# Kernel optimization log

Hardware: AMD Instinct MI355X
Metric: run time of the kernel (lower is better)

## Reference

```python
import jax, jax.numpy as jnp
import numpy as np

T, B, P, D = 64, 32, 9, 512  # turns, batch, parties(=N_s), D_u=D_k=D_h


def setup_inputs() -> dict:
    key = jax.random.key(0)
    ks = jax.random.split(key, 12)
    f = lambda k, s: jax.random.normal(k, s, dtype=jnp.float32)
    sc = 0.02
    spk = jax.random.randint(ks[5], (T, B), 0, P)
    return {
        "U": f(ks[0], (T, B, D)), "SK": f(ks[1], (T, B, D)),
        "NU": f(ks[2], (T, B, D)), "LK": f(ks[3], (T, B, D)),
        "A": f(ks[4], (T, B, D)),
        "qmask": jax.nn.one_hot(spk, P, dtype=jnp.float32),  # one-hot party mask [T,B,P]
        # 4 Attention blocks (state11,state12,state21,state22): w_k, w_q, proj (D->D each)
        "Wk": f(ks[6], (4, D, D)) * sc, "bk": jnp.zeros((4, D), jnp.float32),
        "Wq": f(ks[7], (4, D, D)) * sc, "bq": jnp.zeros((4, D), jnp.float32),
        "Wp": f(ks[8], (4, D, D)) * sc, "bp": jnp.zeros((4, D), jnp.float32),
        # per-speaker GRUCell weights (dict of GRUCells -> stacked [P, ...], torch gate order r,z,n)
        "Wih": f(ks[9], (P, 3 * D, D)) * sc, "Whh": f(ks[10], (P, 3 * D, D)) * sc,
        "bih": jnp.zeros((P, 3 * D), jnp.float32), "bhh": jnp.zeros((P, 3 * D), jnp.float32),
    }


def reference(U, SK, NU, LK, A, qmask, Wk, bk, Wq, bq, Wp, bp, Wih, Whh, bih, bhh):
    Tn, Bn, Dn = U.shape
    Pn = qmask.shape[-1]
    bidx = jnp.arange(Bn)

    def attn(i, k2, q2):
        # Attention(D_k), n_head=1, score_function='dot_product', dropout=0 (eval)
        kx = k2 @ Wk[i].T + bk[i]                 # [B, D]
        qx = q2 @ Wq[i].T + bq[i]                 # [B, D]
        # k_len=q_len=1 -> score = <qx_b, kx_b>; original softmaxes over dim=0 (the batch axis!)
        score = jax.nn.softmax(jnp.sum(qx * kx, axis=-1), axis=0)  # [B]
        return (score[:, None] * kx) @ Wp[i].T + bp[i]  # [B, D]

    def gru(x, h, idx):
        # dynamically-routed per-speaker GRUCell: gather speaker weights, batched matvec
        gi = jnp.einsum('bd,bkd->bk', x, Wih[idx]) + bih[idx]  # [B, 3D]
        gh = jnp.einsum('bd,bkd->bk', h, Whh[idx]) + bhh[idx]
        ir, iz, inn = jnp.split(gi, 3, axis=-1)
        hr, hz, hn = jnp.split(gh, 3, axis=-1)
        r = jax.nn.sigmoid(ir + hr)
        z = jax.nn.sigmoid(iz + hz)
        n = jnp.tanh(inn + r * hn)
        return (1.0 - z) * n + z * h

    # qmask_n[t] = qmask[t+1] (next speaker), last repeats
    qmask_n = jnp.concatenate([qmask[1:], qmask[-1:]], axis=0)

    def step(s, xs):
        u, sk, nu, lk, qm, qmn = xs
        qi = jnp.argmax(qm, axis=1)   # speaker id per sample
        qni = jnp.argmax(qmn, axis=1)  # listener (next speaker) id
        s0s = s[bidx, qi]              # _select_parties
        s0l = s[bidx, qni]
        s_0 = attn(0, sk, u)
        s_s = attn(1, sk, s_0)
        s_1 = attn(2, lk, nu)
        s_l = attn(3, lk, s_1)
        spk = gru(s_s, s0s, qi)        # speaker state update
        lst = gru(s_l, s0l, qni)       # listener state update
        s_full = jnp.zeros_like(s).at[bidx, qi].set(spk)   # scatter_ dim=1
        l_full = jnp.zeros_like(s).at[bidx, qni].set(lst)
        s_new = (s * (1.0 - qm[..., None] - qmn[..., None])
                 + s_full * qm[..., None] + l_full * qmn[..., None])
        return s_new, s_new[bidx, qi]  # emit selected speaker state

    s0 = jnp.zeros((Bn, Pn, Dn), U.dtype)
    _, outs = jax.lax.scan(step, s0, (U, SK, NU, LK, qmask, qmask_n))
    # s_ starts as zeros(1, B, D_h) and concatenates per-step selections -> [T+1, B, D]
    return jnp.concatenate([jnp.zeros((1, Bn, Dn), U.dtype), outs], axis=0)
```

## Files before the change

kernel.cpp:

```cpp
#include <hip/hip_runtime.h>
#include <math.h>

#define Tn 64
#define Bn 32
#define Pn 9
#define Dn 512
#define TBn 2048
#define G3 1536
#define NCH 16
#define DD2 262144

using short8 = __attribute__((ext_vector_type(8))) short;
using f32x4  = __attribute__((ext_vector_type(4))) float;
typedef unsigned long long ull;
typedef unsigned int uint;

__device__ __forceinline__ float fsigmoid(float x){ return 1.0f/(1.0f+__expf(-x)); }
__device__ __forceinline__ ushort f2bf(float x){
  unsigned u = __float_as_uint(x);
  return (ushort)((u + 0x7FFFu + ((u>>16)&1u)) >> 16);
}
__device__ __forceinline__ float bf2f(ushort h){
  return __uint_as_float(((unsigned)h)<<16);
}
__device__ __forceinline__ uint pk32(float x){
  ushort h = f2bf(x);
  ushort l = f2bf(x - bf2f(h));
  return ((uint)h << 16) | (uint)l;
}

__device__ __forceinline__ ull ld_agent8(const ull* p){
  return __hip_atomic_load(p, __ATOMIC_RELAXED, __HIP_MEMORY_SCOPE_AGENT);
}
__device__ __forceinline__ void st_agent8(ull* p, ull v){
  __hip_atomic_store(p, v, __ATOMIC_RELAXED, __HIP_MEMORY_SCOPE_AGENT);
}
__device__ __forceinline__ unsigned ld_agent4(const int* p){
  return (unsigned)__hip_atomic_load(p, __ATOMIC_RELAXED, __HIP_MEMORY_SCOPE_AGENT);
}
__device__ __forceinline__ void st_agent4(int* p, int v){
  __hip_atomic_store(p, v, __ATOMIC_RELAXED, __HIP_MEMORY_SCOPE_AGENT);
}
__device__ __forceinline__ float ulo(ull v){ return __uint_as_float((unsigned)v); }
__device__ __forceinline__ float uhi(ull v){ return __uint_as_float((unsigned)(v>>32)); }
__device__ __forceinline__ ull upack(float a, float b){
  return ((ull)__float_as_uint(b) << 32) | (ull)__float_as_uint(a);
}
__device__ __forceinline__ float wave_red(float a){
  a += __shfl_xor(a, 1);  a += __shfl_xor(a, 2);  a += __shfl_xor(a, 4);
  a += __shfl_xor(a, 8);  a += __shfl_xor(a, 16); a += __shfl_xor(a, 32);
  return a;
}

__global__ void k_prep(const float* __restrict__ qmask, int* __restrict__ qi,
                       int* __restrict__ qni, float* __restrict__ h0A,
                       float* __restrict__ h0B, float* __restrict__ out,
                       int* __restrict__ counts, int* __restrict__ lists,
                       int* __restrict__ dcnt, int* __restrict__ dlist,
                       int* __restrict__ rowflag){
  int t = blockIdx.x; int tid = threadIdx.x;
  int gidx = blockIdx.x*256 + tid;
  if (gidx < 16) counts[gidx] = 0;
  if (gidx < Bn*Pn*NCH) st_agent4(&rowflag[gidx], 0);
  for (int i=gidx; i<9*4096; i+=64*256) lists[i] = -1;
  __shared__ int qis[32], qnis[32];
  __shared__ int cnt9[9];
  if (tid < 9) cnt9[tid] = 0;
  if (tid < Bn){
    int b = tid;
    const float* qm = qmask + ((size_t)t*Bn + b)*Pn;
    int best = 0; float bv = qm[0];
    #pragma unroll
    for (int p=1;p<Pn;p++){ float v=qm[p]; if (v>bv){bv=v;best=p;} }
    qi[t*Bn+b] = best; qis[b] = best;
    int tn = (t==Tn-1)? t : t+1;
    const float* qmn = qmask + ((size_t)tn*Bn + b)*Pn;
    best = 0; bv = qmn[0];
    #pragma unroll
    for (int p=1;p<Pn;p++){ float v=qmn[p]; if (v>bv){bv=v;best=p;} }
    qni[t*Bn+b] = best; qnis[b] = best;
  }
  __syncthreads();
  if (tid < Bn){
    int sp = qis[tid], lp = qnis[tid];
    if (sp == lp){
      int i = atomicAdd(&cnt9[sp], 1);
      dlist[(t*9+sp)*32 + i] = tid | 256 | 512;
    } else {
      int i = atomicAdd(&cnt9[sp], 1);
      dlist[(t*9+sp)*32 + i] = tid | 256;
      int j = atomicAdd(&cnt9[lp], 1);
      dlist[(t*9+lp)*32 + j] = tid | 512;
    }
  }
  __syncthreads();
  if (tid < 9) dcnt[t*9+tid] = cnt9[tid];
  for (int i=tid; i<2304; i+=256){ h0A[t*2304 + i] = 0.f; h0B[t*2304 + i] = 0.f; }
  for (int i=tid; i<256;  i+=256) out[t*256 + i] = 0.f;
}

__global__ __launch_bounds__(256) void k_aux(
    const int* __restrict__ qi, const int* __restrict__ qni,
    int* __restrict__ counts, int* __restrict__ lists,
    const int* __restrict__ dcnt, int* __restrict__ dlist,
    const float* __restrict__ Wq, const float* __restrict__ Wih,
    const float* __restrict__ Wp, const float* __restrict__ bp,
    const float* __restrict__ bq, const float* __restrict__ bih,
    ushort* __restrict__ WpTpk, float* __restrict__ cvec,
    float* __restrict__ C1, float* __restrict__ C3){
  int bx = blockIdx.x, tid = threadIdx.x;
  if (bx < 16){
    int id = bx*256 + tid;
    int role = id >> 11, tb = id & (TBn-1);
    int p = role ? qni[tb] : qi[tb];
    int slot = atomicAdd(&counts[p], 1);
    lists[p*4096 + slot] = id;
  } else if (bx == 16){
    for (int idx = tid; idx < Bn*Pn; idx += 256){
      int b = idx / Pn, pp = idx % Pn;
      int v = 0;
      for (int t=0;t<Tn;t++){
        if (qi[t*Bn+b]==pp || qni[t*Bn+b]==pp){
          int nn = dcnt[t*9+pp];
          int base = (t*9+pp)*32;
          for (int i=0;i<nn;i++){
            if ((dlist[base+i] & 31) == b){ dlist[base+i] |= (v<<16); break; }
          }
          v++;
        }
      }
    }
  } else if (bx < 33){
    int g = (bx-17)*256 + tid;
    int r = g >> 3, cb = (g & 7)*64;
    #pragma unroll
    for (int mi=0; mi<2; mi++){
      const float* src = Wp + (size_t)mi*2*DD2;
      ushort* dst = WpTpk + (size_t)(mi*512 + r)*1024;
      for (int c=cb; c<cb+64; c++){
        float v = src[(size_t)c*512 + r];
        ushort h = f2bf(v);
        dst[c] = h; dst[512+c] = f2bf(v - bf2f(h));
      }
    }
  } else {
    int wv = (bx-33)*4 + (tid>>6), lane = tid & 63;
    if (wv < 16){
      for (int i=0;i<64;i++){
        int r = wv*64 + i;
        int m = r >> 9, j = r & 511;
        const float* wrow = Wq + (size_t)(m?3:1)*DD2 + (size_t)j*512;
        const float* bpv  = bp + (m? 1024 : 0);
        float acc = 0.f;
        #pragma unroll
        for (int e=0;e<8;e++) acc = fmaf(wrow[lane*8+e], bpv[lane*8+e], acc);
        acc = wave_red(acc);
        if (lane==0) cvec[r] = acc + bq[(m?1536:512) + j];
      }
    } else if (wv < 232){
      int base = (wv-16)*64;
      for (int i=0;i<64;i++){
        int r = base + i;
        const float* wrow = Wih + (size_t)r*512;
        float a1=0.f, a3=0.f;
        #pragma unroll
        for (int e=0;e<8;e++){
          float wv8 = wrow[lane*8+e];
          a1 = fmaf(wv8, bp[512 + lane*8+e], a1);
          a3 = fmaf(wv8, bp[1536 + lane*8+e], a3);
        }
        a1 = wave_red(a1); a3 = wave_red(a3);
        if (lane==0){ C1[r] = a1 + bih[r]; C3[r] = a3 + bih[r]; }
      }
    }
  }
}

struct PkD { const float* s; ushort* d; int n; };
__global__ __launch_bounds__(256) void k_packB(PkD p0, PkD p1, PkD p2, PkD p3,
                                               PkD p4, PkD p5, PkD p6, PkD p7){
  PkD D;
  switch (blockIdx.z){
    case 0: D=p0; break; case 1: D=p1; break; case 2: D=p2; break; case 3: D=p3; break;
    case 4: D=p4; break; case 5: D=p5; break; case 6: D=p6; break; default: D=p7; break;
  }
  int total = D.n * 128;
  for (int idx = blockIdx.x*256 + threadIdx.x; idx < total; idx += gridDim.x*256){
    int r = idx >> 7, c4 = idx & 127;
    float4 v = ((const float4*)D.s)[idx];
    ushort h0=f2bf(v.x), h1=f2bf(v.y), h2=f2bf(v.z), h3=f2bf(v.w);
    ushort l0=f2bf(v.x-bf2f(h0)), l1=f2bf(v.y-bf2f(h1)),
           l2=f2bf(v.z-bf2f(h2)), l3=f2bf(v.w-bf2f(h3));
    ushort* base = D.d + (size_t)r*1024;
    *(ushort4*)(base + c4*4)       = make_ushort4(h0,h1,h2,h3);
    *(ushort4*)(base + 512 + c4*4) = make_ushort4(l0,l1,l2,l3);
  }
}

struct MMd {
  const ushort* A; const ushort* B; float* C; const float* bias; ushort* Cpk;
  int asr, ahi, alo, bsr, bhi, blo, ldc, gx;
};
__global__ __launch_bounds__(256) void k_mmB(MMd d0, MMd d1, MMd d2, MMd d3){
  MMd d;
  switch (blockIdx.z){
    case 0: d=d0; break; case 1: d=d1; break; case 2: d=d2; break; default: d=d3; break;
  }
  if ((int)blockIdx.x >= d.gx) return;
  __shared__ ushort AshH[64*64];
  __shared__ ushort AshL[64*64];
  __shared__ ushort BshH[64*64];
  __shared__ ushort BshL[64*64];
  int bm = blockIdx.y*64, bn = blockIdx.x*64;
  int tid = threadIdx.x;
  int lane = tid & 63, w = tid >> 6;
  int wm = (w>>1)*32, wn = (w&1)*32;
  f32x4 acc[2][2] = {};
  int r0 = tid >> 3, g0 = tid & 7;
  int r1 = r0 + 32;
  const ushort* Ah = d.A + d.ahi;
  const ushort* Al = d.A + d.alo;
  const ushort* Bh = d.B + d.bhi;
  const ushort* Bl = d.B + d.blo;
  for (int k0=0; k0<512; k0+=64){
    short8 vah0 = *(const short8*)(Ah + (size_t)(bm+r0)*d.asr + k0 + g0*8);
    short8 vah1 = *(const short8*)(Ah + (size_t)(bm+r1)*d.asr + k0 + g0*8);
    short8 val0 = *(const short8*)(Al + (size_t)(bm+r0)*d.asr + k0 + g0*8);
    short8 val1 = *(const short8*)(Al + (size_t)(bm+r1)*d.asr + k0 + g0*8);
    short8 vbh0 = *(const short8*)(Bh + (size_t)(bn+r0)*d.bsr + k0 + g0*8);
    short8 vbh1 = *(const short8*)(Bh + (size_t)(bn+r1)*d.bsr + k0 + g0*8);
    short8 vbl0 = *(const short8*)(Bl + (size_t)(bn+r0)*d.bsr + k0 + g0*8);
    short8 vbl1 = *(const short8*)(Bl + (size_t)(bn+r1)*d.bsr + k0 + g0*8);
    __syncthreads();
    *(short8*)(AshH + r0*64 + ((g0 ^ (r0&7))*8)) = vah0;
    *(short8*)(AshH + r1*64 + ((g0 ^ (r1&7))*8)) = vah1;
    *(short8*)(AshL + r0*64 + ((g0 ^ (r0&7))*8)) = val0;
    *(short8*)(AshL + r1*64 + ((g0 ^ (r1&7))*8)) = val1;
    *(short8*)(BshH + r0*64 + ((g0 ^ (r0&7))*8)) = vbh0;
    *(short8*)(BshH + r1*64 + ((g0 ^ (r1&7))*8)) = vbh1;
    *(short8*)(BshL + r0*64 + ((g0 ^ (r0&7))*8)) = vbl0;
    *(short8*)(BshL + r1*64 + ((g0 ^ (r1&7))*8)) = vbl1;
    __syncthreads();
    #pragma unroll
    for (int kk=0; kk<2; ++kk){
      int gs = kk*4 + (lane>>4);
      short8 afh[2], afl[2], bfh[2], bfl[2];
      #pragma unroll
      for (int mi=0; mi<2; ++mi){
        int row = wm + mi*16 + (lane&15);
        afh[mi] = *(const short8*)(AshH + row*64 + ((gs ^ (row&7))*8));
        afl[mi] = *(const short8*)(AshL + row*64 + ((gs ^ (row&7))*8));
      }
      #pragma unroll
      for (int ni=0; ni<2; ++ni){
        int row = wn + ni*16 + (lane&15);
        bfh[ni] = *(const short8*)(BshH + row*64 + ((gs ^ (row&7))*8));
        bfl[ni] = *(const short8*)(BshL + row*64 + ((gs ^ (row&7))*8));
      }
      #pragma unroll
      for (int mi=0; mi<2; ++mi)
        #pragma unroll
        for (int ni=0; ni<2; ++ni){
          acc[mi][ni] = __builtin_amdgcn_mfma_f32_16x16x32_bf16(afh[mi], bfh[ni], acc[mi][ni], 0,0,0);
          acc[mi][ni] = __builtin_amdgcn_mfma_f32_16x16x32_bf16(afh[mi], bfl[ni], acc[mi][ni], 0,0,0);
          acc[mi][ni] = __builtin_amdgcn_mfma_f32_16x16x32_bf16(afl[mi], bfh[ni], acc[mi][ni], 0,0,0);
        }
    }
  }
  #pragma unroll
  for (int mi=0; mi<2; ++mi){
    #pragma unroll
    for (int ni=0; ni<2; ++ni){
      #pragma unroll
      for (int i=0;i<4;i++){
        int row = bm + wm + mi*16 + (lane>>4)*4 + i;
        int col = bn + wn + ni*16 + (lane&15);
        float v = acc[mi][ni][i];
        if (d.bias) v += d.bias[col];
        if (d.C) d.C[(size_t)row*d.ldc + col] = v;
        if (d.Cpk){
          ushort h = f2bf(v);
          d.Cpk[(size_t)row*2*d.ldc + col] = h;
          d.Cpk[(size_t)row*2*d.ldc + d.ldc + col] = f2bf(v - bf2f(h));
        }
      }
    }
  }
}

__global__ __launch_bounds__(256) void k_mm_g(
    const ushort* __restrict__ Spk0, const ushort* __restrict__ Spk1,
    const ushort* __restrict__ Wihpk,
    const int* __restrict__ counts, const int* __restrict__ lists,
    float* __restrict__ gis, float* __restrict__ gil)
{
  int p = blockIdx.z;
  int mt = blockIdx.y;
  if (mt*64 >= counts[p]) return;
  int bn = blockIdx.x*64;
  __shared__ ushort AshH[64*64];
  __shared__ ushort AshL[64*64];
  __shared__ ushort BshH[64*64];
  __shared__ ushort BshL[64*64];
  __shared__ int rid[64];
  int tid = threadIdx.x;
  int lane = tid & 63, w = tid >> 6;
  int wm = (w>>1)*32, wn = (w&1)*32;
  if (tid < 64) rid[tid] = lists[p*4096 + mt*64 + tid];
  __syncthreads();
  f32x4 acc[2][2] = {};
  int r0 = tid >> 3, g0 = tid & 7;
  int r1 = r0 + 32;
  int id0 = rid[r0], id1 = rid[r1];
  const ushort* As0 = (id0 >= 0) ? (((id0>>11)? Spk1:Spk0) + (size_t)(id0 & (TBn-1))*1024) : nullptr;
  const ushort* As1 = (id1 >= 0) ? (((id1>>11)? Spk1:Spk0) + (size_t)(id1 & (TBn-1))*1024) : nullptr;
  const ushort* Wb  = Wihpk + (size_t)(p*G3 + bn)*1024;
  short8 zz = {0,0,0,0,0,0,0,0};
  for (int k0=0; k0<512; k0+=64){
    short8 vah0 = As0 ? *(const short8*)(As0 + k0 + g0*8)       : zz;
    short8 val0 = As0 ? *(const short8*)(As0 + 512 + k0 + g0*8) : zz;
    short8 vah1 = As1 ? *(const short8*)(As1 + k0 + g0*8)       : zz;
    short8 val1 = As1 ? *(const short8*)(As1 + 512 + k0 + g0*8) : zz;
    short8 vbh0 = *(const short8*)(Wb + (size_t)r0*1024 + k0 + g0*8);
    short8 vbl0 = *(const short8*)(Wb + (size_t)r0*1024 + 512 + k0 + g0*8);
    short8 vbh1 = *(const short8*)(Wb + (size_t)r1*1024 + k0 + g0*8);
    short8 vbl1 = *(const short8*)(Wb + (size_t)r1*1024 + 512 + k0 + g0*8);
    __syncthreads();
    *(short8*)(AshH + r0*64 + ((g0 ^ (r0&7))*8)) = vah0;
    *(short8*)(AshH + r1*64 + ((g0 ^ (r1&7))*8)) = vah1;
    *(short8*)(AshL + r0*64 + ((g0 ^ (r0&7))*8)) = val0;
    *(short8*)(AshL + r1*64 + ((g0 ^ (r1&7))*8)) = val1;
    *(short8*)(BshH + r0*64 + ((g0 ^ (r0&7))*8)) = vbh0;
    *(short8*)(BshH + r1*64 + ((g0 ^ (r1&7))*8)) = vbh1;
    *(short8*)(BshL + r0*64 + ((g0 ^ (r0&7))*8)) = vbl0;
    *(short8*)(BshL + r1*64 + ((g0 ^ (r1&7))*8)) = vbl1;
    __syncthreads();
    #pragma unroll
    for (int kk=0; kk<2; ++kk){
      int gs = kk*4 + (lane>>4);
      short8 afh[2], afl[2], bfh[2], bfl[2];
      #pragma unroll
      for (int mi=0; mi<2; ++mi){
        int row = wm + mi*16 + (lane&15);
        afh[mi] = *(const short8*)(AshH + row*64 + ((gs ^ (row&7))*8));
        afl[mi] = *(const short8*)(AshL + row*64 + ((gs ^ (row&7))*8));
      }
      #pragma unroll
      for (int ni=0; ni<2; ++ni){
        int row = wn + ni*16 + (lane&15);
        bfh[ni] = *(const short8*)(BshH + row*64 + ((gs ^ (row&7))*8));
        bfl[ni] = *(const short8*)(BshL + row*64 + ((gs ^ (row&7))*8));
      }
      #pragma unroll
      for (int mi=0; mi<2; ++mi)
        #pragma unroll
        for (int ni=0; ni<2; ++ni){
          acc[mi][ni] = __builtin_amdgcn_mfma_f32_16x16x32_bf16(afh[mi], bfh[ni], acc[mi][ni], 0,0,0);
          acc[mi][ni] = __builtin_amdgcn_mfma_f32_16x16x32_bf16(afh[mi], bfl[ni], acc[mi][ni], 0,0,0);
          acc[mi][ni] = __builtin_amdgcn_mfma_f32_16x16x32_bf16(afl[mi], bfh[ni], acc[mi][ni], 0,0,0);
        }
    }
  }
  #pragma unroll
  for (int mi=0; mi<2; ++mi){
    #pragma unroll
    for (int ni=0; ni<2; ++ni){
      #pragma unroll
      for (int i=0;i<4;i++){
        int lrow2 = wm + mi*16 + (lane>>4)*4 + i;
        int id = rid[lrow2];
        if (id < 0) continue;
        int col = bn + wn + ni*16 + (lane&15);
        float* dst = ((id>>11) ? gil : gis) + (size_t)(id & (TBn-1))*G3;
        dst[col] = acc[mi][ni][i];
      }
    }
  }
}

__global__ __launch_bounds__(256) void k_scoreT(
    const float* __restrict__ qx0, const ushort* __restrict__ kxA,
    const float* __restrict__ qq1,
    const float* __restrict__ qx2, const ushort* __restrict__ kxB,
    const float* __restrict__ qq3,
    const float* __restrict__ cvec, float* __restrict__ scS,
    float* __restrict__ scL){
  int t = blockIdx.x, side = blockIdx.y, tid = threadIdx.x;
  const float* qx; const ushort* kx; const float* qq; const float* cv; float* sco;
  if (side==0){ qx=qx0; kx=kxA; qq=qq1; cv=cvec;     sco=scS; }
  else        { qx=qx2; kx=kxB; qq=qq3; cv=cvec+512; sco=scL; }
  __shared__ float p0[256], pA[256], pB[256];
  __shared__ float d0s[32], dAs[32], dBs[32], es[32], e1[32];
  int b = tid>>3, j = tid&7;
  const float* q   = qx + (size_t)(t*Bn+b)*Dn;
  const float* qqr = qq + (size_t)(t*Bn+b)*Dn;
  const ushort* kr = kx + (size_t)(t*Bn+b)*2048;
  float s0=0.f, sA=0.f, sB=0.f;
  for (int d=j; d<Dn; d+=8){
    float k0v = bf2f(kr[d])     + bf2f(kr[1024+d]);
    float k1v = bf2f(kr[512+d]) + bf2f(kr[1536+d]);
    s0 = fmaf(q[d],   k0v, s0);
    sA = fmaf(qqr[d], k1v, sA);
    sB = fmaf(cv[d],  k1v, sB);
  }
  p0[tid]=s0; pA[tid]=sA; pB[tid]=sB;
  __syncthreads();
  if (tid < 32){
    float a0=0,aA=0,aB=0;
    #pragma unroll
    for (int jj=0;jj<8;jj++){ a0+=p0[tid*8+jj]; aA+=pA[tid*8+jj]; aB+=pB[tid*8+jj]; }
    d0s[tid]=a0; dAs[tid]=aA; dBs[tid]=aB;
  }
  __syncthreads();
  if (tid < 32){
    float mx=d0s[0]; for(int o=1;o<32;o++) mx=fmaxf(mx,d0s[o]);
    es[tid]=__expf(d0s[tid]-mx);
  }
  __syncthreads();
  if (tid < 32){
    float sum=0; for(int o=0;o<32;o++) sum+=es[o];
    float sc0 = es[tid]/sum;
    e1[tid] = fmaf(sc0, dAs[tid], dBs[tid]);
  }
  __syncthreads();
  if (tid < 32){
    float mx=e1[0]; for(int o=1;o<32;o++) mx=fmaxf(mx,e1[o]);
    es[tid]=__expf(e1[tid]-mx);
  }
  __syncthreads();
  if (tid < 32){
    float sum=0; for(int o=0;o<32;o++) sum+=es[o];
    sco[t*Bn+tid] = es[tid]/sum;
  }
}

#define DC 32
#define NT 6
__global__ __launch_bounds__(512, 1) void k_rec(
    float* hA, float* hB,
    const int* __restrict__ dcnt, const int* __restrict__ dlist,
    const float* __restrict__ Whh, const float* __restrict__ bhh,
    const float* __restrict__ gis, const float* __restrict__ gil,
    const float* __restrict__ scS, const float* __restrict__ scL,
    const float* __restrict__ C1, const float* __restrict__ C3,
    float* __restrict__ out, int* rowflag){
  int p  = blockIdx.x;
  int ci = blockIdx.y;
  int d0 = ci * DC;
  int tid = threadIdx.x;
  int wave = tid >> 6, lane = tid & 63;

  __shared__ float4 hsh4[16][130];
  __shared__ uint   ab16[16][516];
  __shared__ float  ghs[16][97];
  __shared__ int    dls[32];
  __shared__ float  scSsh[TBn], scLsh[TBn];

  for (int i=tid; i<TBn; i+=512){ scSsh[i]=scS[i]; scLsh[i]=scL[i]; }

  short8 Bh[16], Bl[16];
  if (wave < NT){
    int wrow = wave*16 + (lane & 15);
    int grow = (wrow >> 5)*Dn + d0 + (wrow & 31);
    const float* wsrc = Whh + ((size_t)p*G3 + grow)*Dn + (lane>>4)*8;
    #pragma unroll
    for (int ks=0; ks<16; ++ks){
      float4 w0 = *(const float4*)(wsrc + ks*32);
      float4 w1 = *(const float4*)(wsrc + ks*32 + 4);
      float xs[8] = {w0.x,w0.y,w0.z,w0.w,w1.x,w1.y,w1.z,w1.w};
      #pragma unroll
      for (int j=0;j<8;j++){
        ushort hh = f2bf(xs[j]);
        Bh[ks][j] = (short)hh;
        Bl[ks][j] = (short)f2bf(xs[j] - bf2f(hh));
      }
    }
  }
  int dd0 = (tid & 15)*2, dfix = d0 + dd0;
  float bhr0 = bhh[p*G3 + dfix],        bhr1 = bhh[p*G3 + dfix + 1];
  float bhz0 = bhh[p*G3 + Dn + dfix],   bhz1 = bhh[p*G3 + Dn + dfix + 1];
  float bhn0 = bhh[p*G3 + 2*Dn + dfix], bhn1 = bhh[p*G3 + 2*Dn + dfix + 1];
  float c1v[6], c3v[6];
  {
    const float* C1p = C1 + p*G3; const float* C3p = C3 + p*G3;
    c1v[0]=C1p[dfix];        c1v[1]=C1p[dfix+1];
    c1v[2]=C1p[Dn+dfix];     c1v[3]=C1p[Dn+dfix+1];
    c1v[4]=C1p[2*Dn+dfix];   c1v[5]=C1p[2*Dn+dfix+1];
    c3v[0]=C3p[dfix];        c3v[1]=C3p[dfix+1];
    c3v[2]=C3p[Dn+dfix];     c3v[3]=C3p[Dn+dfix+1];
    c3v[4]=C3p[2*Dn+dfix];   c3v[5]=C3p[2*Dn+dfix+1];
  }

  int entC = 0;
  if (tid < 32) entC = dlist[(0*9 + p)*32 + tid];

  for (int t=0; t<Tn; ++t){
    __syncthreads();
    if (tid < 32) dls[tid] = entC;
    __syncthreads();
    if (t+1 < Tn && tid < 32) entC = dlist[((t+1)*9 + p)*32 + tid];
    int n = dcnt[t*9+p];
    if (!n) continue;

    float pg[12];
    {
      int i = tid >> 4;
      if (i < n && i < 16){
        int ent = dls[i]; int b = ent & 31;
        if (ent & 256){
          const float* gS = gis + (size_t)(t*Bn + b)*G3;
          pg[0]=gS[dfix]; pg[1]=gS[dfix+1]; pg[2]=gS[Dn+dfix]; pg[3]=gS[Dn+dfix+1];
          pg[4]=gS[2*Dn+dfix]; pg[5]=gS[2*Dn+dfix+1];
        }
        if (ent & 512){
          const float* gL = gil + (size_t)(t*Bn + b)*G3;
          pg[6]=gL[dfix]; pg[7]=gL[dfix+1]; pg[8]=gL[Dn+dfix]; pg[9]=gL[Dn+dfix+1];
          pg[10]=gL[2*Dn+dfix]; pg[11]=gL[2*Dn+dfix+1];
        }
      }
    }

    {
      int i0 = wave*4 + (lane >> 4);
      if (i0 < n){
        int ent = dls[i0];
        unsigned need = (unsigned)(ent >> 16);
        if (need){
          int b = ent & 31;
          const int* cell = &rowflag[(b*Pn + p)*NCH + (lane & 15)];
          while (ld_agent4(cell) < need) __builtin_amdgcn_s_sleep(1);
        }
      }
    }
    __syncthreads();

    for (int g0=0; g0<n; g0+=16){
      int gn = n - g0; if (gn > 16) gn = 16;
      for (int idx=tid; idx<gn*128; idx+=512){
        int r = idx >> 7, q = idx & 127;
        int ent = dls[g0+r];
        int b = ent & 31;
        const float* hsrc = ((ent>>16) & 1) ? hB : hA;
        const ull* src = (const ull*)(hsrc + ((size_t)b*Pn + p)*Dn) + q*2;
        ull v0 = ld_agent8(src), v1 = ld_agent8(src+1);
        float4 f; f.x = ulo(v0); f.y = uhi(v0); f.z = ulo(v1); f.w = uhi(v1);
        hsh4[r][q ^ ((q>>3)&7)] = f;
        uint4 pk; pk.x = pk32(f.x); pk.y = pk32(f.y); pk.z = pk32(f.z); pk.w = pk32(f.w);
        *(uint4*)&ab16[r][q*4] = pk;
      }
      __syncthreads();

      if (wave < NT){
        f32x4 acc = {0.f,0.f,0.f,0.f};
        int arow = lane & 15;
        int kq   = (lane >> 4)*8;
        #pragma unroll
        for (int ks=0; ks<16; ++ks){
          uint4 u0 = *(const uint4*)&ab16[arow][ks*32 + kq];
          uint4 u1 = *(const uint4*)&ab16[arow][ks*32 + kq + 4];
          uint uu[8] = {u0.x,u0.y,u0.z,u0.w,u1.x,u1.y,u1.z,u1.w};
          short8 Ah, Al;
          #pragma unroll
          for (int j=0;j<8;j++){
            Ah[j] = (short)(uu[j] >> 16);
            Al[j] = (short)(uu[j] & 0xffffu);
          }
          acc = __builtin_amdgcn_mfma_f32_16x16x32_bf16(Ah, Bh[ks], acc, 0,0,0);
          acc = __builtin_amdgcn_mfma_f32_16x16x32_bf16(Ah, Bl[ks], acc, 0,0,0);
          acc = __builtin_amdgcn_mfma_f32_16x16x32_bf16(Al, Bh[ks], acc, 0,0,0);
        }
        #pragma unroll
        for (int i=0;i<4;i++)
          ghs[(lane>>4)*4 + i][wave*16 + (lane & 15)] = acc[i];
      }
      __syncthreads();

      if (tid < gn*16){
        int i = tid >> 4;
        int ent = dls[g0+i];
        int b = ent & 31;
        bool S = (ent & 256) != 0, L = (ent & 512) != 0;
        int v = ent >> 16;
        float* hdst = (v & 1) ? hA : hB;
        int qq = dfix >> 2;
        float4 u = hsh4[i][qq ^ ((qq>>3)&7)];
        float hv0 = (dfix & 2) ? u.z : u.x;
        float hv1 = (dfix & 2) ? u.w : u.y;
        float ghr0 = ghs[i][dd0]    + bhr0, ghr1 = ghs[i][dd0+1]    + bhr1;
        float ghz0 = ghs[i][32+dd0] + bhz0, ghz1 = ghs[i][32+dd0+1] + bhz1;
        float ghn0 = ghs[i][64+dd0] + bhn0, ghn1 = ghs[i][64+dd0+1] + bhn1;
        float v0 = hv0, v1 = hv1;
        if (S){
          float g0v,g1v,g2v,g3v,g4v,g5v;
          if (g0 == 0){ g0v=pg[0]; g1v=pg[1]; g2v=pg[2]; g3v=pg[3]; g4v=pg[4]; g5v=pg[5]; }
          else {
            const float* gS = gis + (size_t)(t*Bn + b)*G3;
            g0v=gS[dfix]; g1v=gS[dfix+1]; g2v=gS[Dn+dfix]; g3v=gS[Dn+dfix+1];
            g4v=gS[2*Dn+dfix]; g5v=gS[2*Dn+dfix+1];
          }
          float sc = scSsh[t*Bn + b];
          float i0 = fmaf(sc, g0v, c1v[0]), i1 = fmaf(sc, g1v, c1v[1]);
          float i2 = fmaf(sc, g2v, c1v[2]), i3 = fmaf(sc, g3v, c1v[3]);
          float i4 = fmaf(sc, g4v, c1v[4]), i5 = fmaf(sc, g5v, c1v[5]);
          float rg0 = fsigmoid(i0 + ghr0), rg1 = fsigmoid(i1 + ghr1);
          float zg0 = fsigmoid(i2 + ghz0), zg1 = fsigmoid(i3 + ghz1);
          float ng0 = tanhf(fmaf(rg0, ghn0, i4));
          float ng1 = tanhf(fmaf(rg1, ghn1, i5));
          v0 = fmaf(zg0, hv0 - ng0, ng0);
          v1 = fmaf(zg1, hv1 - ng1, ng1);
        }
        if (L){
          float g0v,g1v,g2v,g3v,g4v,g5v;
          if (g0 == 0){ g0v=pg[6]; g1v=pg[7]; g2v=pg[8]; g3v=pg[9]; g4v=pg[10]; g5v=pg[11]; }
          else {
            const float* gL = gil + (size_t)(t*Bn + b)*G3;
            g0v=gL[dfix]; g1v=gL[dfix+1]; g2v=gL[Dn+dfix]; g3v=gL[Dn+dfix+1];
            g4v=gL[2*Dn+dfix]; g5v=gL[2*Dn+dfix+1];
          }
          float sc = scLsh[t*Bn + b];
          float i0 = fmaf(sc, g0v, c3v[0]), i1 = fmaf(sc, g1v, c3v[1]);
          float i2 = fmaf(sc, g2v, c3v[2]), i3 = fmaf(sc, g3v, c3v[3]);
          float i4 = fmaf(sc, g4v, c3v[4]), i5 = fmaf(sc, g5v, c3v[5]);
          float rg0 = fsigmoid(i0 + ghr0), rg1 = fsigmoid(i1 + ghr1);
          float zg0 = fsigmoid(i2 + ghz0), zg1 = fsigmoid(i3 + ghz1);
          float ng0 = tanhf(fmaf(rg0, ghn0, i4));
          float ng1 = tanhf(fmaf(rg1, ghn1, i5));
          float hl0 = fmaf(zg0, hv0 - ng0, ng0);
          float hl1 = fmaf(zg1, hv1 - ng1, ng1);
          if (S){ v0 += hl0 - hv0; v1 += hl1 - hv1; }
          else  { v0 = hl0; v1 = hl1; }
        }
        st_agent8((ull*)(hdst + ((size_t)b*Pn + p)*Dn + dfix), upack(v0, v1));
        if (S) *(ull*)(out + ((size_t)(t+1)*Bn + b)*Dn + dfix) = upack(v0, v1);
      }
      __syncthreads();
    }

    if (tid < n){
      int ent = dls[tid];
      st_agent4(&rowflag[((ent & 31)*Pn + p)*NCH + ci], (ent >> 16) + 1);
    }
  }
}

extern "C" void kernel_launch(void* const* d_in, const int* in_sizes, int n_in,
                              void* d_out, int out_size, void* d_ws, size_t ws_size,
                              hipStream_t stream){
  const float* U    = (const float*)d_in[0];
  const float* SK   = (const float*)d_in[1];
  const float* NU   = (const float*)d_in[2];
  const float* LK   = (const float*)d_in[3];
  const float* qmask= (const float*)d_in[5];
  const float* bk   = (const float*)d_in[7];
  const float* bq   = (const float*)d_in[9];
  const float* bp   = (const float*)d_in[11];
  const float* Wk   = (const float*)d_in[6];
  const float* Wq   = (const float*)d_in[8];
  const float* Wp   = (const float*)d_in[10];
  const float* Wih  = (const float*)d_in[12];
  const float* Whh  = (const float*)d_in[13];
  const float* bih  = (const float*)d_in[14];
  const float* bhh  = (const float*)d_in[15];
  float* out = (float*)d_out;

  char* w = (char*)d_ws;
  size_t off = 0;
  auto alloc = [&](size_t bytes)->void*{ void* p = w + off; off += (bytes + 255) & ~(size_t)255; return p; };
  ushort* SKpk  = (ushort*)alloc(2048UL*1024*2);
  ushort* LKpk  = (ushort*)alloc(2048UL*1024*2);
  ushort* Upk   = (ushort*)alloc(2048UL*1024*2);
  ushort* NUpk  = (ushort*)alloc(2048UL*1024*2);
  ushort* Wkpk  = (ushort*)alloc(2048UL*1024*2);
  ushort* Wqpk  = (ushort*)alloc(2048UL*1024*2);
  ushort* Wppk  = (ushort*)alloc(2048UL*1024*2);
  ushort* Wihpk = (ushort*)alloc(13824UL*1024*2);
  ushort* WpTpk = (ushort*)alloc(1024UL*1024*2);
  ushort* WWpk  = (ushort*)alloc(1024UL*1024*2);
  ushort* kxApk = (ushort*)alloc(2048UL*2048*2);
  ushort* kxBpk = (ushort*)alloc(2048UL*2048*2);
  ushort* pkx1pk= (ushort*)alloc(2048UL*1024*2);
  ushort* pkx3pk= (ushort*)alloc(2048UL*1024*2);
  float* qxA    = (float*)alloc(2048UL*512*4);
  float* qxB    = (float*)alloc(2048UL*512*4);
  float* qq1    = (float*)alloc(2048UL*512*4);
  float* qq3    = (float*)alloc(2048UL*512*4);
  float* gis    = (float*)alloc(2048UL*1536*4);
  float* gil    = (float*)alloc(2048UL*1536*4);
  float* hA     = (float*)alloc(32UL*9*512*4);
  float* hB     = (float*)alloc(32UL*9*512*4);
  float* cvec   = (float*)alloc(1024*4);
  float* C1     = (float*)alloc(9UL*1536*4);
  float* C3     = (float*)alloc(9UL*1536*4);
  float* scS    = (float*)alloc(2048*4);
  float* scL    = (float*)alloc(2048*4);
  int* qi       = (int*)alloc(2048*4);
  int* qni      = (int*)alloc(2048*4);
  int* counts   = (int*)alloc(16*4);
  int* lists    = (int*)alloc(9*4096*4);
  int* dcnt     = (int*)alloc(64*9*4);
  int* dlist    = (int*)alloc(64*9*32*4);
  int* rowflag  = (int*)alloc(32*9*NCH*4);
  (void)ws_size; (void)in_sizes; (void)n_in; (void)out_size;

  dim3 blk(256);

  k_prep<<<64, blk, 0, stream>>>(qmask, qi, qni, hA, hB, out, counts, lists, dcnt, dlist, rowflag);
  k_aux <<<91, blk, 0, stream>>>(qi, qni, counts, lists, dcnt, dlist,
                                 Wq, Wih, Wp, bp, bq, bih, WpTpk, cvec, C1, C3);

  {
    PkD p0{SK, SKpk, 2048}, p1{LK, LKpk, 2048}, p2{U, Upk, 2048}, p3{NU, NUpk, 2048};
    PkD p4{Wk, Wkpk, 2048}, p5{Wq, Wqpk, 2048}, p6{Wp, Wppk, 2048}, p7{Wih, Wihpk, 13824};
    k_packB<<<dim3(256,1,8), blk, 0, stream>>>(p0,p1,p2,p3,p4,p5,p6,p7);
  }

  {
    MMd d0{Wqpk+(size_t)512*1024,  WpTpk,                 nullptr, nullptr, WWpk,
           1024,0,512, 1024,0,512, 512, 8};
    MMd d1{Wqpk+(size_t)1536*1024, WpTpk+(size_t)512*1024, nullptr, nullptr, WWpk+(size_t)512*1024,
           1024,0,512, 1024,0,512, 512, 8};
    k_mmB<<<dim3(8,8,2), blk, 0, stream>>>(d0,d1,d0,d0);
  }

  {
    MMd d0{SKpk, Wkpk,                   nullptr, bk,      kxApk, 1024,0,512, 1024,0,512, 1024, 16};
    MMd d1{LKpk, Wkpk+(size_t)1024*1024, nullptr, bk+1024, kxBpk, 1024,0,512, 1024,0,512, 1024, 16};
    MMd d2{Upk,  Wqpk,                   qxA,     bq,      nullptr,1024,0,512, 1024,0,512, 512,  8};
    MMd d3{NUpk, Wqpk+(size_t)1024*1024, qxB,     bq+1024, nullptr,1024,0,512, 1024,0,512, 512,  8};
    k_mmB<<<dim3(16,32,4), blk, 0, stream>>>(d0,d1,d2,d3);
  }

  {
    MMd d0{kxApk, Wppk+(size_t)512*1024,  nullptr, nullptr, pkx1pk, 2048,512,1536, 1024,0,512, 512, 8};
    MMd d1{kxBpk, Wppk+(size_t)1536*1024, nullptr, nullptr, pkx3pk, 2048,512,1536, 1024,0,512, 512, 8};
    MMd d2{kxApk, WWpk,                   qq1,     nullptr, nullptr,2048,0,  1024, 1024,0,512, 512, 8};
    MMd d3{kxBpk, WWpk+(size_t)512*1024,  qq3,     nullptr, nullptr,2048,0,  1024, 1024,0,512, 512, 8};
    k_mmB<<<dim3(8,32,4), blk, 0, stream>>>(d0,d1,d2,d3);
  }

  k_mm_g<<<dim3(24,64,9), blk, 0, stream>>>(pkx1pk, pkx3pk, Wihpk, counts, lists, gis, gil);

  k_scoreT<<<dim3(64,2), blk, 0, stream>>>(qxA, kxApk, qq1, qxB, kxBpk, qq3, cvec, scS, scL);

  k_rec<<<dim3(9,NCH), dim3(512), 0, stream>>>(hA, hB, dcnt, dlist, Whh, bhh,
                                               gis, gil, scS, scL, C1, C3, out, rowflag);
}
```

Baseline: 653.9 us.

## Fuse activation bf16 split-packing into GEMM loads and widen aux bias precompute

Adds a GEMM variant that reads fp32 activations (SK, LK, U, NU) directly and splits them into bf16 hi/lo pairs in registers while loading tiles. This removes the separate packing pass and its workspace round-trip for those four inputs. The aux kernel's bias-folding matvecs now use one wave per row across thousands of blocks instead of 64 rows per wave over a few blocks, which raises parallelism at the cost of more block launches. The conversion is now redone by each column-block tile, so the same work is repeated redundantly.

Result: slower. 667.0 us (+2.0%).

```diff
diff --git a/kernel.cpp b/kernel.cpp
--- a/kernel.cpp
+++ b/kernel.cpp
@@ -144,45 +144,39 @@
       }
     }
   } else {
-    int wv = (bx-33)*4 + (tid>>6), lane = tid & 63;
-    if (wv < 16){
-      for (int i=0;i<64;i++){
-        int r = wv*64 + i;
-        int m = r >> 9, j = r & 511;
-        const float* wrow = Wq + (size_t)(m?3:1)*DD2 + (size_t)j*512;
-        const float* bpv  = bp + (m? 1024 : 0);
-        float acc = 0.f;
-        #pragma unroll
-        for (int e=0;e<8;e++) acc = fmaf(wrow[lane*8+e], bpv[lane*8+e], acc);
-        acc = wave_red(acc);
-        if (lane==0) cvec[r] = acc + bq[(m?1536:512) + j];
-      }
-    } else if (wv < 232){
-      int base = (wv-16)*64;
-      for (int i=0;i<64;i++){
-        int r = base + i;
-        const float* wrow = Wih + (size_t)r*512;
-        float a1=0.f, a3=0.f;
-        #pragma unroll
-        for (int e=0;e<8;e++){
-          float wv8 = wrow[lane*8+e];
-          a1 = fmaf(wv8, bp[512 + lane*8+e], a1);
-          a3 = fmaf(wv8, bp[1536 + lane*8+e], a3);
-        }
-        a1 = wave_red(a1); a3 = wave_red(a3);
-        if (lane==0){ C1[r] = a1 + bih[r]; C3[r] = a3 + bih[r]; }
-      }
+    int wid = tid >> 6, lane = tid & 63;
+    int wv = (bx-33)*4 + wid;
+    if (wv < 9*G3){
+      int r = wv;
+      const float* wrow = Wih + (size_t)r*512;
+      float a1=0.f, a3=0.f;
+      #pragma unroll
+      for (int e=0;e<8;e++){
+        float wv8 = wrow[lane*8+e];
+        a1 = fmaf(wv8, bp[512 + lane*8+e], a1);
+        a3 = fmaf(wv8, bp[1536 + lane*8+e], a3);
+      }
+      a1 = wave_red(a1); a3 = wave_red(a3);
+      if (lane==0){ C1[r] = a1 + bih[r]; C3[r] = a3 + bih[r]; }
+    } else if (wv < 9*G3 + 1024){
+      int r = wv - 9*G3;
+      int m = r >> 9, j = r & 511;
+      const float* wrow = Wq + (size_t)(m?3:1)*DD2 + (size_t)j*512;
+      const float* bpv  = bp + (m? 1024 : 0);
+      float acc = 0.f;
+      #pragma unroll
+      for (int e=0;e<8;e++) acc = fmaf(wrow[lane*8+e], bpv[lane*8+e], acc);
+      acc = wave_red(acc);
+      if (lane==0) cvec[r] = acc + bq[(m?1536:512) + j];
     }
   }
 }
 
 struct PkD { const float* s; ushort* d; int n; };
-__global__ __launch_bounds__(256) void k_packB(PkD p0, PkD p1, PkD p2, PkD p3,
-                                               PkD p4, PkD p5, PkD p6, PkD p7){
+__global__ __launch_bounds__(256) void k_packB(PkD p0, PkD p1, PkD p2, PkD p3){
   PkD D;
   switch (blockIdx.z){
-    case 0: D=p0; break; case 1: D=p1; break; case 2: D=p2; break; case 3: D=p3; break;
-    case 4: D=p4; break; case 5: D=p5; break; case 6: D=p6; break; default: D=p7; break;
+    case 0: D=p0; break; case 1: D=p1; break; case 2: D=p2; break; default: D=p3; break;
   }
   int total = D.n * 128;
   for (int idx = blockIdx.x*256 + threadIdx.x; idx < total; idx += gridDim.x*256){
@@ -227,6 +221,108 @@
     short8 vah1 = *(const short8*)(Ah + (size_t)(bm+r1)*d.asr + k0 + g0*8);
     short8 val0 = *(const short8*)(Al + (size_t)(bm+r0)*d.asr + k0 + g0*8);
     short8 val1 = *(const short8*)(Al + (size_t)(bm+r1)*d.asr + k0 + g0*8);
+    short8 vbh0 = *(const short8*)(Bh + (size_t)(bn+r0)*d.bsr + k0 + g0*8);
+    short8 vbh1 = *(const short8*)(Bh + (size_t)(bn+r1)*d.bsr + k0 + g0*8);
+    short8 vbl0 = *(const short8*)(Bl + (size_t)(bn+r0)*d.bsr + k0 + g0*8);
+    short8 vbl1 = *(const short8*)(Bl + (size_t)(bn+r1)*d.bsr + k0 + g0*8);
+    __syncthreads();
+    *(short8*)(AshH + r0*64 + ((g0 ^ (r0&7))*8)) = vah0;
+    *(short8*)(AshH + r1*64 + ((g0 ^ (r1&7))*8)) = vah1;
+    *(short8*)(AshL + r0*64 + ((g0 ^ (r0&7))*8)) = val0;
+    *(short8*)(AshL + r1*64 + ((g0 ^ (r1&7))*8)) = val1;
+    *(short8*)(BshH + r0*64 + ((g0 ^ (r0&7))*8)) = vbh0;
+    *(short8*)(BshH + r1*64 + ((g0 ^ (r1&7))*8)) = vbh1;
+    *(short8*)(BshL + r0*64 + ((g0 ^ (r0&7))*8)) = vbl0;
+    *(short8*)(BshL + r1*64 + ((g0 ^ (r1&7))*8)) = vbl1;
+    __syncthreads();
+    #pragma unroll
+    for (int kk=0; kk<2; ++kk){
+      int gs = kk*4 + (lane>>4);
+      short8 afh[2], afl[2], bfh[2], bfl[2];
+      #pragma unroll
+      for (int mi=0; mi<2; ++mi){
+        int row = wm + mi*16 + (lane&15);
+        afh[mi] = *(const short8*)(AshH + row*64 + ((gs ^ (row&7))*8));
+        afl[mi] = *(const short8*)(AshL + row*64 + ((gs ^ (row&7))*8));
+      }
+      #pragma unroll
+      for (int ni=0; ni<2; ++ni){
+        int row = wn + ni*16 + (lane&15);
+        bfh[ni] = *(const short8*)(BshH + row*64 + ((gs ^ (row&7))*8));
+        bfl[ni] = *(const short8*)(BshL + row*64 + ((gs ^ (row&7))*8));
+      }
+      #pragma unroll
+      for (int mi=0; mi<2; ++mi)
+        #pragma unroll
+        for (int ni=0; ni<2; ++ni){
+          acc[mi][ni] = __builtin_amdgcn_mfma_f32_16x16x32_bf16(afh[mi], bfh[ni], acc[mi][ni], 0,0,0);
+          acc[mi][ni] = __builtin_amdgcn_mfma_f32_16x16x32_bf16(afh[mi], bfl[ni], acc[mi][ni], 0,0,0);
+          acc[mi][ni] = __builtin_amdgcn_mfma_f32_16x16x32_bf16(afl[mi], bfh[ni], acc[mi][ni], 0,0,0);
+        }
+    }
+  }
+  #pragma unroll
+  for (int mi=0; mi<2; ++mi){
+    #pragma unroll
+    for (int ni=0; ni<2; ++ni){
+      #pragma unroll
+      for (int i=0;i<4;i++){
+        int row = bm + wm + mi*16 + (lane>>4)*4 + i;
+        int col = bn + wn + ni*16 + (lane&15);
+        float v = acc[mi][ni][i];
+        if (d.bias) v += d.bias[col];
+        if (d.C) d.C[(size_t)row*d.ldc + col] = v;
+        if (d.Cpk){
+          ushort h = f2bf(v);
+          d.Cpk[(size_t)row*2*d.ldc + col] = h;
+          d.Cpk[(size_t)row*2*d.ldc + d.ldc + col] = f2bf(v - bf2f(h));
+        }
+      }
+    }
+  }
+}
+
+struct MMf {
+  const float* A; const ushort* B; float* C; const float* bias; ushort* Cpk;
+  int asr, bsr, bhi, blo, ldc, gx;
+};
+__global__ __launch_bounds__(256) void k_mmF(MMf d0, MMf d1, MMf d2, MMf d3){
+  MMf d;
+  switch (blockIdx.z){
+    case 0: d=d0; break; case 1: d=d1; break; case 2: d=d2; break; default: d=d3; break;
+  }
+  if ((int)blockIdx.x >= d.gx) return;
+  __shared__ ushort AshH[64*64];
+  __shared__ ushort AshL[64*64];
+  __shared__ ushort BshH[64*64];
+  __shared__ ushort BshL[64*64];
+  int bm = blockIdx.y*64, bn = blockIdx.x*64;
+  int tid = threadIdx.x;
+  int lane = tid & 63, w = tid >> 6;
+  int wm = (w>>1)*32, wn = (w&1)*32;
+  f32x4 acc[2][2] = {};
+  int r0 = tid >> 3, g0 = tid & 7;
+  int r1 = r0 + 32;
+  const ushort* Bh = d.B + d.bhi;
+  const ushort* Bl = d.B + d.blo;
+  for (int k0=0; k0<512; k0+=64){
+    float4 a00 = *(const float4*)(d.A + (size_t)(bm+r0)*d.asr + k0 + g0*8);
+    float4 a01 = *(const float4*)(d.A + (size_t)(bm+r0)*d.asr + k0 + g0*8 + 4);
+    float4 a10 = *(const float4*)(d.A + (size_t)(bm+r1)*d.asr + k0 + g0*8);
+    float4 a11 = *(const float4*)(d.A + (size_t)(bm+r1)*d.asr + k0 + g0*8 + 4);
+    short8 vah0, val0, vah1, val1;
+    {
+      float xs[8] = {a00.x,a00.y,a00.z,a00.w,a01.x,a01.y,a01.z,a01.w};
+      #pragma unroll
+      for (int j=0;j<8;j++){
+        ushort h = f2bf(xs[j]); vah0[j] = (short)h; val0[j] = (short)f2bf(xs[j]-bf2f(h));
+      }
+      float ys[8] = {a10.x,a10.y,a10.z,a10.w,a11.x,a11.y,a11.z,a11.w};
+      #pragma unroll
+      for (int j=0;j<8;j++){
+        ushort h = f2bf(ys[j]); vah1[j] = (short)h; val1[j] = (short)f2bf(ys[j]-bf2f(h));
+      }
+    }
     short8 vbh0 = *(const short8*)(Bh + (size_t)(bn+r0)*d.bsr + k0 + g0*8);
     short8 vbh1 = *(const short8*)(Bh + (size_t)(bn+r1)*d.bsr + k0 + g0*8);
     short8 vbl0 = *(const short8*)(Bl + (size_t)(bn+r0)*d.bsr + k0 + g0*8);
@@ -666,10 +762,6 @@
   char* w = (char*)d_ws;
   size_t off = 0;
   auto alloc = [&](size_t bytes)->void*{ void* p = w + off; off += (bytes + 255) & ~(size_t)255; return p; };
-  ushort* SKpk  = (ushort*)alloc(2048UL*1024*2);
-  ushort* LKpk  = (ushort*)alloc(2048UL*1024*2);
-  ushort* Upk   = (ushort*)alloc(2048UL*1024*2);
-  ushort* NUpk  = (ushort*)alloc(2048UL*1024*2);
   ushort* Wkpk  = (ushort*)alloc(2048UL*1024*2);
   ushort* Wqpk  = (ushort*)alloc(2048UL*1024*2);
   ushort* Wppk  = (ushort*)alloc(2048UL*1024*2);
@@ -705,17 +797,16 @@
   dim3 blk(256);
 
   k_prep<<<64, blk, 0, stream>>>(qmask, qi, qni, hA, hB, out, counts, lists, dcnt, dlist, rowflag);
-  k_aux <<<91, blk, 0, stream>>>(qi, qni, counts, lists, dcnt, dlist,
-                                 Wq, Wih, Wp, bp, bq, bih, WpTpk, cvec, C1, C3);
+  k_aux <<<33 + 3712, blk, 0, stream>>>(qi, qni, counts, lists, dcnt, dlist,
+                                        Wq, Wih, Wp, bp, bq, bih, WpTpk, cvec, C1, C3);
 
   {
-    PkD p0{SK, SKpk, 2048}, p1{LK, LKpk, 2048}, p2{U, Upk, 2048}, p3{NU, NUpk, 2048};
-    PkD p4{Wk, Wkpk, 2048}, p5{Wq, Wqpk, 2048}, p6{Wp, Wppk, 2048}, p7{Wih, Wihpk, 13824};
-    k_packB<<<dim3(256,1,8), blk, 0, stream>>>(p0,p1,p2,p3,p4,p5,p6,p7);
+    PkD p0{Wk, Wkpk, 2048}, p1{Wq, Wqpk, 2048}, p2{Wp, Wppk, 2048}, p3{Wih, Wihpk, 13824};
+    k_packB<<<dim3(256,1,4), blk, 0, stream>>>(p0,p1,p2,p3);
   }
 
   {
-    MMd d0{Wqpk+(size_t)512*1024,  WpTpk,                 nullptr, nullptr, WWpk,
+    MMd d0{Wqpk+(size_t)512*1024,  WpTpk,                  nullptr, nullptr, WWpk,
            1024,0,512, 1024,0,512, 512, 8};
     MMd d1{Wqpk+(size_t)1536*1024, WpTpk+(size_t)512*1024, nullptr, nullptr, WWpk+(size_t)512*1024,
            1024,0,512, 1024,0,512, 512, 8};
@@ -723,11 +814,11 @@
   }
 
   {
-    MMd d0{SKpk, Wkpk,                   nullptr, bk,      kxApk, 1024,0,512, 1024,0,512, 1024, 16};
-    MMd d1{LKpk, Wkpk+(size_t)1024*1024, nullptr, bk+1024, kxBpk, 1024,0,512, 1024,0,512, 1024, 16};
-    MMd d2{Upk,  Wqpk,                   qxA,     bq,      nullptr,1024,0,512, 1024,0,512, 512,  8};
-    MMd d3{NUpk, Wqpk+(size_t)1024*1024, qxB,     bq+1024, nullptr,1024,0,512, 1024,0,512, 512,  8};
-    k_mmB<<<dim3(16,32,4), blk, 0, stream>>>(d0,d1,d2,d3);
+    MMf d0{SK, Wkpk,                   nullptr, bk,      kxApk, 512, 1024,0,512, 1024, 16};
+    MMf d1{LK, Wkpk+(size_t)1024*1024, nullptr, bk+1024, kxBpk, 512, 1024,0,512, 1024, 16};
+    MMf d2{U,  Wqpk,                   qxA,     bq,      nullptr,512, 1024,0,512, 512,  8};
+    MMf d3{NU, Wqpk+(size_t)1024*1024, qxB,     bq+1024, nullptr,512, 1024,0,512, 512,  8};
+    k_mmF<<<dim3(16,32,4), blk, 0, stream>>>(d0,d1,d2,d3);
   }
 
   {
```
